# Kernel tuning notes

Measured on AMD Instinct MI355X. Metric: run time of the kernel, lower is better.

The kernel has to match this reference:

```python
import jax, jax.numpy as jnp
import numpy as np

H, D, BS = 32, 128, 64          # num_heads, head_dim, gate block_size
GATE_DIM = 64
GATE_TEMP = 2.0                 # _GATE_TARGET_TEMPERATURE
CLAMP_MIN, CLAMP_MAX = -50.0, 50.0


def _rotate_half(x):
    x1, x2 = jnp.split(x, 2, axis=-1)
    return jnp.concatenate([-x2, x1], axis=-1)


def setup_inputs() -> dict:
    key = jax.random.key(0)
    ks = jax.random.split(key, 8)
    B, S, E = 1, 2048, 4096
    hidden_states = jax.random.normal(ks[0], (B, S, E), jnp.float32) * 0.02
    # standard RoPE tables, [B, S, D]
    inv_freq = 1.0 / (10000.0 ** (jnp.arange(0, D, 2, dtype=jnp.float32) / D))
    freqs = jnp.arange(S, dtype=jnp.float32)[:, None] * inv_freq[None, :]
    emb = jnp.concatenate([freqs, freqs], axis=-1)
    cos = jnp.broadcast_to(jnp.cos(emb)[None], (B, S, D)).astype(jnp.float32)
    sin = jnp.broadcast_to(jnp.sin(emb)[None], (B, S, D)).astype(jnp.float32)
    Wq = jax.random.normal(ks[1], (E, E), jnp.float32) * 0.02
    Wk = jax.random.normal(ks[2], (E, E), jnp.float32) * 0.02
    Wv = jax.random.normal(ks[3], (E, E), jnp.float32) * 0.02
    Wo = jax.random.normal(ks[4], (E, E), jnp.float32) * 0.02
    Wg_q = jax.random.normal(ks[5], (GATE_DIM, D), jnp.float32) * 0.05
    Wg_k = jax.random.normal(ks[6], (GATE_DIM, D), jnp.float32) * 0.05
    return {"hidden_states": hidden_states, "cos": cos, "sin": sin,
            "Wq": Wq, "Wk": Wk, "Wv": Wv, "Wo": Wo,
            "Wg_q": Wg_q, "Wg_k": Wg_k}


def reference(hidden_states, cos, sin, Wq, Wk, Wv, Wo, Wg_q, Wg_k):
    B, S, E = hidden_states.shape
    scale = np.float32(1.0 / np.sqrt(D))

    # ---- base attention (training path: full dense attention w/ scores) ----
    q = (hidden_states @ Wq.T).reshape(B, S, H, D).transpose(0, 2, 1, 3)  # [B,H,S,D]
    k = (hidden_states @ Wk.T).reshape(B, S, H, D).transpose(0, 2, 1, 3)
    v = (hidden_states @ Wv.T).reshape(B, S, H, D).transpose(0, 2, 1, 3)

    # _apply_rotary_pos_emb: cos/sin are 3D [B,S,D] -> unsqueeze head dim
    c, s = cos[:, None], sin[:, None]
    q = q * c + _rotate_half(q) * s
    k = k * c + _rotate_half(k) * s

    scores = jnp.einsum('bhqd,bhkd->bhqk', q, k) * scale  # [B,H,S,S]
    causal = jnp.tril(jnp.ones((S, S), dtype=bool))
    scores = jnp.where(causal, scores, -jnp.inf)
    attn = jax.nn.softmax(scores, axis=-1)
    ctx = jnp.einsum('bhqk,bhkd->bhqd', attn, v)
    attn_output = ctx.transpose(0, 2, 1, 3).reshape(B, S, E) @ Wo.T

    # ---- _compute_gate_target: blockwise maxpool -> clamp -> tempered softmax ----
    NB = S // BS  # S divisible by BS, so the -inf padding branch is a no-op
    block_max = scores.reshape(B, H, NB, BS, NB, BS).max(axis=(3, 5))  # [B,H,NB,NB]
    finite = jnp.isfinite(block_max)
    block_max = jnp.where(finite, jnp.clip(block_max, CLAMP_MIN, CLAMP_MAX), block_max)
    gate_target = jax.nn.softmax(
        block_max.reshape(B, H, NB * NB) / GATE_TEMP, axis=-1
    ).reshape(B, H, NB, NB)

    # ---- AttnGate prediction: mean-pooled block Q/K -> low-rank block logits ----
    qb = q.reshape(B, H, NB, BS, D).mean(axis=3)  # [B,H,NB,D]
    kb = k.reshape(B, H, NB, BS, D).mean(axis=3)
    gq = jnp.einsum('bhnd,gd->bhng', qb, Wg_q)
    gk = jnp.einsum('bhnd,gd->bhng', kb, Wg_k)
    glogits = jnp.einsum('bhqg,bhkg->bhqk', gq, gk) * np.float32(1.0 / np.sqrt(GATE_DIM))
    bmask = jnp.tril(jnp.ones((NB, NB), dtype=bool))  # block-causal
    glogits = jnp.where(bmask, glogits, -jnp.inf)
    gate_pred = jax.nn.softmax(
        glogits.reshape(B, H, NB * NB), axis=-1
    ).reshape(B, H, NB, NB)

    return attn_output, gate_pred, gate_target
```

## Files before the change

### kernel.cpp

```cpp
#include <hip/hip_runtime.h>
#include <stdint.h>

#define S_LEN 2048
#define EMB   4096
#define NHEAD 32
#define DHEAD 128
#define NBLK  32
#define GDIM  64

typedef float  f32x4  __attribute__((ext_vector_type(4)));
typedef __bf16 bf16x8 __attribute__((ext_vector_type(8)));
typedef unsigned short u16;

__device__ __forceinline__ u16 f2bf(float f) {
  uint32_t u = __float_as_uint(f);
  u += 0x7fffu + ((u >> 16) & 1u);
  return (u16)(u >> 16);
}
__device__ __forceinline__ float bf2f(u16 u) {
  return __uint_as_float(((uint32_t)u) << 16);
}

__device__ __forceinline__ void ld_lds16(const u16* g, u16* l) {
  __builtin_amdgcn_global_load_lds((const __attribute__((address_space(1))) void*)g,
                                   (__attribute__((address_space(3))) void*)l, 16, 0, 0);
}

__global__ void conv_f32_bf16(const float* __restrict__ in, u16* __restrict__ out, int n4) {
  int i = blockIdx.x * 256 + threadIdx.x;
  if (i >= n4) return;
  float4 v = ((const float4*)in)[i];
  ushort4 o;
  o.x = f2bf(v.x); o.y = f2bf(v.y); o.z = f2bf(v.z); o.w = f2bf(v.w);
  ((ushort4*)out)[i] = o;
}

template<int MODE>
__global__ void __launch_bounds__(256, 2) gemm_bt(
    const u16* __restrict__ A, const u16* __restrict__ B, void* __restrict__ outp,
    const float* __restrict__ cosp, const float* __restrict__ sinp)
{
  __shared__ u16 lA[128 * 32];
  __shared__ u16 lB[128 * 32];
  __shared__ u16 lT[MODE == 1 ? 128 * 136 : 1];

  const int tid = threadIdx.x;
  const int w = tid >> 6, lane = tid & 63;
  const int r = lane & 15, qd = lane >> 4;
  const int m0 = blockIdx.y * 128, n0 = blockIdx.x * 128;
  const int K = EMB;

  f32x4 acc[2][8];
#pragma unroll
  for (int mi = 0; mi < 2; ++mi)
#pragma unroll
    for (int ni = 0; ni < 8; ++ni) acc[mi][ni] = (f32x4){0.f, 0.f, 0.f, 0.f};

  const u16* Ab = A + (size_t)(m0 + w * 16 + (lane >> 2)) * K + (lane & 3) * 8;
  const u16* Bb = B + (size_t)(n0 + w * 16 + (lane >> 2)) * K + (lane & 3) * 8;
  u16* lAb = &lA[(w * 16) * 32];
  u16* lBb = &lB[(w * 16) * 32];

  for (int k0 = 0; k0 < K; k0 += 32) {
    __syncthreads();
    ld_lds16(Ab + k0, lAb);
    ld_lds16(Ab + (size_t)64 * K + k0, lAb + 64 * 32);
    ld_lds16(Bb + k0, lBb);
    ld_lds16(Bb + (size_t)64 * K + k0, lBb + 64 * 32);
    __syncthreads();
    bf16x8 af0 = *(const bf16x8*)&lA[(w * 32 + r) * 32 + qd * 8];
    bf16x8 af1 = *(const bf16x8*)&lA[(w * 32 + 16 + r) * 32 + qd * 8];
#pragma unroll
    for (int ni = 0; ni < 8; ++ni) {
      bf16x8 bf = *(const bf16x8*)&lB[(ni * 16 + r) * 32 + qd * 8];
      acc[0][ni] = __builtin_amdgcn_mfma_f32_16x16x32_bf16(af0, bf, acc[0][ni], 0, 0, 0);
      acc[1][ni] = __builtin_amdgcn_mfma_f32_16x16x32_bf16(af1, bf, acc[1][ni], 0, 0, 0);
    }
  }

  if (MODE == 2) {
    float* out = (float*)outp;
#pragma unroll
    for (int mi = 0; mi < 2; ++mi)
#pragma unroll
      for (int ni = 0; ni < 8; ++ni)
#pragma unroll
        for (int rg = 0; rg < 4; ++rg) {
          int srow = m0 + w * 32 + mi * 16 + qd * 4 + rg;
          out[(size_t)srow * EMB + n0 + ni * 16 + r] = acc[mi][ni][rg];
        }
  } else if (MODE == 0) {
    u16* out = (u16*)outp;
    const int h = n0 >> 7;
#pragma unroll
    for (int mi = 0; mi < 2; ++mi)
#pragma unroll
      for (int ni = 0; ni < 4; ++ni)
#pragma unroll
        for (int rg = 0; rg < 4; ++rg) {
          int srow = m0 + w * 32 + mi * 16 + qd * 4 + rg;
          int dlo = ni * 16 + r;
          float c = cosp[srow * DHEAD + dlo];
          float s = sinp[srow * DHEAD + dlo];
          float lo = acc[mi][ni][rg], hi = acc[mi][ni + 4][rg];
          size_t base = ((size_t)h * S_LEN + srow) * DHEAD;
          out[base + dlo]      = f2bf(lo * c - hi * s);
          out[base + dlo + 64] = f2bf(hi * c + lo * s);
        }
  } else {
    u16* out = (u16*)outp;
    const int h = n0 >> 7;
#pragma unroll
    for (int mi = 0; mi < 2; ++mi)
#pragma unroll
      for (int ni = 0; ni < 8; ++ni)
#pragma unroll
        for (int rg = 0; rg < 4; ++rg) {
          int sl = w * 32 + mi * 16 + qd * 4 + rg;
          lT[sl * 136 + ni * 16 + r] = f2bf(acc[mi][ni][rg]);
        }
    __syncthreads();
    const int d = tid >> 1, sh = (tid & 1) * 64;
    size_t obase = ((size_t)h * DHEAD + d) * S_LEN + m0 + sh;
#pragma unroll
    for (int i8 = 0; i8 < 8; ++i8) {
      u16 tmp[8];
#pragma unroll
      for (int j = 0; j < 8; ++j) tmp[j] = lT[(sh + i8 * 8 + j) * 136 + d];
      *(uint4*)&out[obase + i8 * 8] = *(uint4*)tmp;
    }
  }
}

__global__ void __launch_bounds__(256, 2) attn_fwd(
    const u16* __restrict__ qg, const u16* __restrict__ kg, const u16* __restrict__ vtg,
    u16* __restrict__ ctx, float* __restrict__ bmax)
{
  __shared__ u16 lK[64 * 136];
  __shared__ u16 lV[128 * 72];
  __shared__ u16 lP[64 * 72];
  __shared__ float lBM[4 * NBLK];

  const int tid = threadIdx.x;
  const int w = tid >> 6, lane = tid & 63;
  const int r = lane & 15, qd = lane >> 4;
  const int qb = blockIdx.x, h = blockIdx.y;

  bf16x8 qf[4];
  {
    const u16* qp = qg + ((size_t)h * S_LEN + qb * 64 + w * 16 + r) * DHEAD + qd * 8;
#pragma unroll
    for (int ki = 0; ki < 4; ++ki) qf[ki] = *(const bf16x8*)(qp + ki * 32);
  }

  f32x4 o[8];
#pragma unroll
  for (int dt = 0; dt < 8; ++dt) o[dt] = (f32x4){0.f, 0.f, 0.f, 0.f};
  float m_run[4], l_run[4];
#pragma unroll
  for (int rg = 0; rg < 4; ++rg) { m_run[rg] = -__builtin_inff(); l_run[rg] = 0.f; }

  const u16* ksrc = kg + (size_t)h * S_LEN * DHEAD;
  const u16* vsrc = vtg + (size_t)h * DHEAD * S_LEN;
  const float scale = 0.08838834764831845f;

  for (int kb = 0; kb <= qb; ++kb) {
    __syncthreads();
#pragma unroll
    for (int i = 0; i < 4; ++i) {
      int c = tid + 256 * i;
      int row = c >> 4, col = (c & 15) * 8;
      *(uint4*)&lK[row * 136 + col] = *(const uint4*)(ksrc + (size_t)(kb * 64 + row) * DHEAD + col);
    }
#pragma unroll
    for (int i = 0; i < 4; ++i) {
      int c = tid + 256 * i;
      int row = c >> 3, col = (c & 7) * 8;
      *(uint4*)&lV[row * 72 + col] = *(const uint4*)(vsrc + (size_t)row * S_LEN + kb * 64 + col);
    }
    __syncthreads();

    f32x4 sf[4];
#pragma unroll
    for (int nt = 0; nt < 4; ++nt) sf[nt] = (f32x4){0.f, 0.f, 0.f, 0.f};
#pragma unroll
    for (int ki = 0; ki < 4; ++ki)
#pragma unroll
      for (int nt = 0; nt < 4; ++nt) {
        bf16x8 bf = *(const bf16x8*)&lK[(nt * 16 + r) * 136 + ki * 32 + qd * 8];
        sf[nt] = __builtin_amdgcn_mfma_f32_16x16x32_bf16(qf[ki], bf, sf[nt], 0, 0, 0);
      }

    float rmax[4];
#pragma unroll
    for (int rg = 0; rg < 4; ++rg) rmax[rg] = -__builtin_inff();
#pragma unroll
    for (int nt = 0; nt < 4; ++nt)
#pragma unroll
      for (int rg = 0; rg < 4; ++rg) {
        float s = sf[nt][rg] * scale;
        if (kb == qb) {
          int col = nt * 16 + r, row = w * 16 + qd * 4 + rg;
          if (col > row) s = -__builtin_inff();
        }
        sf[nt][rg] = s;
        rmax[rg] = fmaxf(rmax[rg], s);
      }
#pragma unroll
    for (int rg = 0; rg < 4; ++rg) {
      float v = rmax[rg];
      v = fmaxf(v, __shfl_xor(v, 1));
      v = fmaxf(v, __shfl_xor(v, 2));
      v = fmaxf(v, __shfl_xor(v, 4));
      v = fmaxf(v, __shfl_xor(v, 8));
      rmax[rg] = v;
    }
    {
      float v = fmaxf(fmaxf(rmax[0], rmax[1]), fmaxf(rmax[2], rmax[3]));
      v = fmaxf(v, __shfl_xor(v, 16));
      v = fmaxf(v, __shfl_xor(v, 32));
      if (lane == 0) lBM[w * NBLK + kb] = v;
    }

    float alpha[4], rsum[4];
#pragma unroll
    for (int rg = 0; rg < 4; ++rg) {
      float mn = fmaxf(m_run[rg], rmax[rg]);
      alpha[rg] = __expf(m_run[rg] - mn);
      m_run[rg] = mn;
      rsum[rg] = 0.f;
    }
#pragma unroll
    for (int nt = 0; nt < 4; ++nt)
#pragma unroll
      for (int rg = 0; rg < 4; ++rg) {
        float p = __expf(sf[nt][rg] - m_run[rg]);
        sf[nt][rg] = p;
        rsum[rg] += p;
      }
#pragma unroll
    for (int rg = 0; rg < 4; ++rg) {
      float v = rsum[rg];
      v += __shfl_xor(v, 1);
      v += __shfl_xor(v, 2);
      v += __shfl_xor(v, 4);
      v += __shfl_xor(v, 8);
      l_run[rg] = l_run[rg] * alpha[rg] + v;
    }
#pragma unroll
    for (int nt = 0; nt < 4; ++nt)
#pragma unroll
      for (int rg = 0; rg < 4; ++rg)
        lP[(w * 16 + qd * 4 + rg) * 72 + nt * 16 + r] = f2bf(sf[nt][rg]);
#pragma unroll
    for (int dt = 0; dt < 8; ++dt)
#pragma unroll
      for (int rg = 0; rg < 4; ++rg) o[dt][rg] *= alpha[rg];
    bf16x8 pa0 = *(const bf16x8*)&lP[(w * 16 + r) * 72 + qd * 8];
    bf16x8 pa1 = *(const bf16x8*)&lP[(w * 16 + r) * 72 + 32 + qd * 8];
#pragma unroll
    for (int dt = 0; dt < 8; ++dt) {
      bf16x8 bv0 = *(const bf16x8*)&lV[(dt * 16 + r) * 72 + qd * 8];
      bf16x8 bv1 = *(const bf16x8*)&lV[(dt * 16 + r) * 72 + 32 + qd * 8];
      o[dt] = __builtin_amdgcn_mfma_f32_16x16x32_bf16(pa0, bv0, o[dt], 0, 0, 0);
      o[dt] = __builtin_amdgcn_mfma_f32_16x16x32_bf16(pa1, bv1, o[dt], 0, 0, 0);
    }
  }

  float inv[4];
#pragma unroll
  for (int rg = 0; rg < 4; ++rg) inv[rg] = 1.f / l_run[rg];
#pragma unroll
  for (int dt = 0; dt < 8; ++dt)
#pragma unroll
    for (int rg = 0; rg < 4; ++rg) {
      int srow = qb * 64 + w * 16 + qd * 4 + rg;
      ctx[(size_t)srow * EMB + h * DHEAD + dt * 16 + r] = f2bf(o[dt][rg] * inv[rg]);
    }
  __syncthreads();
  if (tid <= qb) {
    float v = fmaxf(fmaxf(lBM[0 * NBLK + tid], lBM[1 * NBLK + tid]),
                    fmaxf(lBM[2 * NBLK + tid], lBM[3 * NBLK + tid]));
    bmax[((size_t)h * NBLK + qb) * NBLK + tid] = v;
  }
}

__global__ void bmean(const u16* __restrict__ x, float* __restrict__ out) {
  int nb = blockIdx.x, h = blockIdx.y, d = threadIdx.x;
  const u16* p = x + ((size_t)h * S_LEN + nb * 64) * DHEAD + d;
  float s = 0.f;
#pragma unroll 8
  for (int i = 0; i < 64; ++i) s += bf2f(p[(size_t)i * DHEAD]);
  out[((size_t)h * NBLK + nb) * DHEAD + d] = s * (1.f / 64.f);
}

__global__ void __launch_bounds__(256) gate_kernel(
    const float* __restrict__ qm, const float* __restrict__ km,
    const float* __restrict__ Wgq, const float* __restrict__ Wgk,
    const float* __restrict__ bmx, float* __restrict__ gpred, float* __restrict__ gtgt)
{
  __shared__ float gq[NBLK * GDIM], gk[NBLK * GDIM];
  __shared__ float red[256];
  const int h = blockIdx.x, tid = threadIdx.x;

  for (int i = 0; i < 8; ++i) {
    int e = tid + 256 * i;
    int n = e >> 6, g = e & 63;
    const float* qrow = qm + ((size_t)h * NBLK + n) * DHEAD;
    const float* krow = km + ((size_t)h * NBLK + n) * DHEAD;
    const float* wq = Wgq + g * DHEAD;
    const float* wk = Wgk + g * DHEAD;
    float s1 = 0.f, s2 = 0.f;
    for (int d = 0; d < DHEAD; ++d) { s1 += qrow[d] * wq[d]; s2 += krow[d] * wk[d]; }
    gq[e] = s1; gk[e] = s2;
  }
  __syncthreads();

  float gl[4];
  for (int i = 0; i < 4; ++i) {
    int idx = tid + 256 * i;
    int qn = idx >> 5, kn = idx & 31;
    if (kn <= qn) {
      float s = 0.f;
      for (int g = 0; g < GDIM; ++g) s += gq[qn * GDIM + g] * gk[kn * GDIM + g];
      gl[i] = s * 0.125f;
    } else gl[i] = -__builtin_inff();
  }
  float mx = fmaxf(fmaxf(gl[0], gl[1]), fmaxf(gl[2], gl[3]));
  red[tid] = mx; __syncthreads();
  for (int st = 128; st > 0; st >>= 1) { if (tid < st) red[tid] = fmaxf(red[tid], red[tid + st]); __syncthreads(); }
  float gmax = red[0]; __syncthreads();
  float ex[4], lsum = 0.f;
  for (int i = 0; i < 4; ++i) { ex[i] = __expf(gl[i] - gmax); lsum += ex[i]; }
  red[tid] = lsum; __syncthreads();
  for (int st = 128; st > 0; st >>= 1) { if (tid < st) red[tid] += red[tid + st]; __syncthreads(); }
  float invs = 1.f / red[0]; __syncthreads();
  for (int i = 0; i < 4; ++i) gpred[(size_t)h * 1024 + tid + 256 * i] = ex[i] * invs;

  float tl[4];
  for (int i = 0; i < 4; ++i) {
    int idx = tid + 256 * i;
    int qn = idx >> 5, kn = idx & 31;
    tl[i] = (kn <= qn) ? fminf(fmaxf(bmx[(size_t)h * 1024 + idx], -50.f), 50.f) * 0.5f
                       : -__builtin_inff();
  }
  float mx2 = fmaxf(fmaxf(tl[0], tl[1]), fmaxf(tl[2], tl[3]));
  red[tid] = mx2; __syncthreads();
  for (int st = 128; st > 0; st >>= 1) { if (tid < st) red[tid] = fmaxf(red[tid], red[tid + st]); __syncthreads(); }
  float tmax = red[0]; __syncthreads();
  float ex2[4], ls2 = 0.f;
  for (int i = 0; i < 4; ++i) { ex2[i] = __expf(tl[i] - tmax); ls2 += ex2[i]; }
  red[tid] = ls2; __syncthreads();
  for (int st = 128; st > 0; st >>= 1) { if (tid < st) red[tid] += red[tid + st]; __syncthreads(); }
  float inv2 = 1.f / red[0];
  for (int i = 0; i < 4; ++i) gtgt[(size_t)h * 1024 + tid + 256 * i] = ex2[i] * inv2;
}

extern "C" void kernel_launch(void* const* d_in, const int* in_sizes, int n_in,
                              void* d_out, int out_size, void* d_ws, size_t ws_size,
                              hipStream_t stream) {
  const float* hidden = (const float*)d_in[0];
  const float* cosp   = (const float*)d_in[1];
  const float* sinp   = (const float*)d_in[2];
  const float* Wq     = (const float*)d_in[3];
  const float* Wk     = (const float*)d_in[4];
  const float* Wv     = (const float*)d_in[5];
  const float* Wo     = (const float*)d_in[6];
  const float* Wgq    = (const float*)d_in[7];
  const float* Wgk    = (const float*)d_in[8];

  char* ws = (char*)d_ws;
  u16*   wbuf = (u16*)ws;
  u16*   hid  = (u16*)(ws + 33554432);
  u16*   qbf  = (u16*)(ws + 50331648);
  u16*   kbf  = (u16*)(ws + 67108864);
  u16*   vtb  = (u16*)(ws + 83886080);
  u16*   ctxb = (u16*)(ws + 100663296);
  float* bmx  = (float*)(ws + 117440512);
  float* qmn  = (float*)(ws + 117571584);
  float* kmn  = (float*)(ws + 118095872);

  float* attn_out = (float*)d_out;
  float* gpred = attn_out + (size_t)S_LEN * EMB;
  float* gtgt  = gpred + NHEAD * NBLK * NBLK;

  conv_f32_bf16<<<8192, 256, 0, stream>>>(hidden, hid, 2097152);

  conv_f32_bf16<<<16384, 256, 0, stream>>>(Wq, wbuf, 4194304);
  gemm_bt<0><<<dim3(32, 16), 256, 0, stream>>>(hid, wbuf, qbf, cosp, sinp);
  conv_f32_bf16<<<16384, 256, 0, stream>>>(Wk, wbuf, 4194304);
  gemm_bt<0><<<dim3(32, 16), 256, 0, stream>>>(hid, wbuf, kbf, cosp, sinp);
  conv_f32_bf16<<<16384, 256, 0, stream>>>(Wv, wbuf, 4194304);
  gemm_bt<1><<<dim3(32, 16), 256, 0, stream>>>(hid, wbuf, vtb, nullptr, nullptr);

  attn_fwd<<<dim3(NBLK, NHEAD), 256, 0, stream>>>(qbf, kbf, vtb, ctxb, bmx);

  conv_f32_bf16<<<16384, 256, 0, stream>>>(Wo, wbuf, 4194304);
  gemm_bt<2><<<dim3(32, 16), 256, 0, stream>>>(ctxb, wbuf, attn_out, nullptr, nullptr);

  bmean<<<dim3(NBLK, NHEAD), 128, 0, stream>>>(qbf, qmn);
  bmean<<<dim3(NBLK, NHEAD), 128, 0, stream>>>(kbf, kmn);
  gate_kernel<<<NHEAD, 256, 0, stream>>>(qmn, kmn, Wgq, Wgk, bmx, gpred, gtgt);
}
```

Measured before the change: 901.8 us.

## Fuse QKV GEMMs, batch weight conversion, pair causal attention blocks

Converts Wq/Wk/Wv in one launch and runs a single QKV GEMM grid of 96x16 tiles instead of three separate GEMMs. This removes serialization and tail effects between the smaller launches. Attention now gives each workgroup query blocks qb and 31-qb, which balances causal work across half as many blocks. The change also pads LDS strides differently, merges the two bmean kernels into one vectorized kernel, and reuses d_out and workspace as scratch for weights. That scratch reuse relies on gemm_out overwriting d_out after the Wv buffer is dead.

After: 790.6 us. -12.3%, faster.

```diff
diff --git a/kernel.cpp b/kernel.cpp
--- a/kernel.cpp
+++ b/kernel.cpp
@@ -35,20 +35,37 @@
   ((ushort4*)out)[i] = o;
 }
 
-template<int MODE>
-__global__ void __launch_bounds__(256, 2) gemm_bt(
-    const u16* __restrict__ A, const u16* __restrict__ B, void* __restrict__ outp,
-    const float* __restrict__ cosp, const float* __restrict__ sinp)
+__global__ void conv3_f32_bf16(const float* __restrict__ a, const float* __restrict__ b,
+                               const float* __restrict__ c, u16* __restrict__ oa,
+                               u16* __restrict__ ob, u16* __restrict__ oc, int n4) {
+  int i = blockIdx.x * 256 + threadIdx.x;
+  if (i >= n4) return;
+  const float* in = (blockIdx.y == 0) ? a : (blockIdx.y == 1) ? b : c;
+  u16* out = (blockIdx.y == 0) ? oa : (blockIdx.y == 1) ? ob : oc;
+  float4 v = ((const float4*)in)[i];
+  ushort4 o;
+  o.x = f2bf(v.x); o.y = f2bf(v.y); o.z = f2bf(v.z); o.w = f2bf(v.w);
+  ((ushort4*)out)[i] = o;
+}
+
+__global__ void __launch_bounds__(256, 2) qkv_gemm(
+    const u16* __restrict__ A, const u16* __restrict__ Bq, const u16* __restrict__ Bk,
+    const u16* __restrict__ Bv, u16* __restrict__ outq, u16* __restrict__ outk,
+    u16* __restrict__ outvt, const float* __restrict__ cosp, const float* __restrict__ sinp)
 {
   __shared__ u16 lA[128 * 32];
   __shared__ u16 lB[128 * 32];
-  __shared__ u16 lT[MODE == 1 ? 128 * 136 : 1];
+  __shared__ u16 lT[128 * 132];
 
   const int tid = threadIdx.x;
   const int w = tid >> 6, lane = tid & 63;
   const int r = lane & 15, qd = lane >> 4;
-  const int m0 = blockIdx.y * 128, n0 = blockIdx.x * 128;
+  const int nb = blockIdx.x;
+  const int which = nb >> 5;
+  const int h = nb & 31;
+  const int m0 = blockIdx.y * 128, n0 = h * 128;
   const int K = EMB;
+  const u16* B = (which == 0) ? Bq : (which == 1) ? Bk : Bv;
 
   f32x4 acc[2][8];
 #pragma unroll
@@ -78,20 +95,8 @@
     }
   }
 
-  if (MODE == 2) {
-    float* out = (float*)outp;
-#pragma unroll
-    for (int mi = 0; mi < 2; ++mi)
-#pragma unroll
-      for (int ni = 0; ni < 8; ++ni)
-#pragma unroll
-        for (int rg = 0; rg < 4; ++rg) {
-          int srow = m0 + w * 32 + mi * 16 + qd * 4 + rg;
-          out[(size_t)srow * EMB + n0 + ni * 16 + r] = acc[mi][ni][rg];
-        }
-  } else if (MODE == 0) {
-    u16* out = (u16*)outp;
-    const int h = n0 >> 7;
+  if (which < 2) {
+    u16* out = which ? outk : outq;
 #pragma unroll
     for (int mi = 0; mi < 2; ++mi)
 #pragma unroll
@@ -108,8 +113,6 @@
           out[base + dlo + 64] = f2bf(hi * c + lo * s);
         }
   } else {
-    u16* out = (u16*)outp;
-    const int h = n0 >> 7;
 #pragma unroll
     for (int mi = 0; mi < 2; ++mi)
 #pragma unroll
@@ -117,7 +120,7 @@
 #pragma unroll
         for (int rg = 0; rg < 4; ++rg) {
           int sl = w * 32 + mi * 16 + qd * 4 + rg;
-          lT[sl * 136 + ni * 16 + r] = f2bf(acc[mi][ni][rg]);
+          lT[sl * 132 + ni * 16 + r] = f2bf(acc[mi][ni][rg]);
         }
     __syncthreads();
     const int d = tid >> 1, sh = (tid & 1) * 64;
@@ -126,172 +129,232 @@
     for (int i8 = 0; i8 < 8; ++i8) {
       u16 tmp[8];
 #pragma unroll
-      for (int j = 0; j < 8; ++j) tmp[j] = lT[(sh + i8 * 8 + j) * 136 + d];
-      *(uint4*)&out[obase + i8 * 8] = *(uint4*)tmp;
-    }
-  }
+      for (int j = 0; j < 8; ++j) tmp[j] = lT[(sh + i8 * 8 + j) * 132 + d];
+      *(uint4*)&outvt[obase + i8 * 8] = *(uint4*)tmp;
+    }
+  }
+}
+
+__global__ void __launch_bounds__(256, 2) gemm_out(
+    const u16* __restrict__ A, const u16* __restrict__ B, float* __restrict__ out)
+{
+  __shared__ u16 lA[128 * 32];
+  __shared__ u16 lB[128 * 32];
+  const int tid = threadIdx.x;
+  const int w = tid >> 6, lane = tid & 63;
+  const int r = lane & 15, qd = lane >> 4;
+  const int m0 = blockIdx.y * 128, n0 = blockIdx.x * 128;
+  const int K = EMB;
+
+  f32x4 acc[2][8];
+#pragma unroll
+  for (int mi = 0; mi < 2; ++mi)
+#pragma unroll
+    for (int ni = 0; ni < 8; ++ni) acc[mi][ni] = (f32x4){0.f, 0.f, 0.f, 0.f};
+
+  const u16* Ab = A + (size_t)(m0 + w * 16 + (lane >> 2)) * K + (lane & 3) * 8;
+  const u16* Bb = B + (size_t)(n0 + w * 16 + (lane >> 2)) * K + (lane & 3) * 8;
+  u16* lAb = &lA[(w * 16) * 32];
+  u16* lBb = &lB[(w * 16) * 32];
+
+  for (int k0 = 0; k0 < K; k0 += 32) {
+    __syncthreads();
+    ld_lds16(Ab + k0, lAb);
+    ld_lds16(Ab + (size_t)64 * K + k0, lAb + 64 * 32);
+    ld_lds16(Bb + k0, lBb);
+    ld_lds16(Bb + (size_t)64 * K + k0, lBb + 64 * 32);
+    __syncthreads();
+    bf16x8 af0 = *(const bf16x8*)&lA[(w * 32 + r) * 32 + qd * 8];
+    bf16x8 af1 = *(const bf16x8*)&lA[(w * 32 + 16 + r) * 32 + qd * 8];
+#pragma unroll
+    for (int ni = 0; ni < 8; ++ni) {
+      bf16x8 bf = *(const bf16x8*)&lB[(ni * 16 + r) * 32 + qd * 8];
+      acc[0][ni] = __builtin_amdgcn_mfma_f32_16x16x32_bf16(af0, bf, acc[0][ni], 0, 0, 0);
+      acc[1][ni] = __builtin_amdgcn_mfma_f32_16x16x32_bf16(af1, bf, acc[1][ni], 0, 0, 0);
+    }
+  }
+#pragma unroll
+  for (int mi = 0; mi < 2; ++mi)
+#pragma unroll
+    for (int ni = 0; ni < 8; ++ni)
+#pragma unroll
+      for (int rg = 0; rg < 4; ++rg) {
+        int srow = m0 + w * 32 + mi * 16 + qd * 4 + rg;
+        out[(size_t)srow * EMB + n0 + ni * 16 + r] = acc[mi][ni][rg];
+      }
 }
 
 __global__ void __launch_bounds__(256, 2) attn_fwd(
     const u16* __restrict__ qg, const u16* __restrict__ kg, const u16* __restrict__ vtg,
     u16* __restrict__ ctx, float* __restrict__ bmax)
 {
-  __shared__ u16 lK[64 * 136];
-  __shared__ u16 lV[128 * 72];
-  __shared__ u16 lP[64 * 72];
+  __shared__ u16 lK[64 * 132];
+  __shared__ u16 lV[128 * 76];
+  __shared__ u16 lP[64 * 76];
   __shared__ float lBM[4 * NBLK];
 
   const int tid = threadIdx.x;
   const int w = tid >> 6, lane = tid & 63;
   const int r = lane & 15, qd = lane >> 4;
-  const int qb = blockIdx.x, h = blockIdx.y;
-
-  bf16x8 qf[4];
-  {
-    const u16* qp = qg + ((size_t)h * S_LEN + qb * 64 + w * 16 + r) * DHEAD + qd * 8;
-#pragma unroll
-    for (int ki = 0; ki < 4; ++ki) qf[ki] = *(const bf16x8*)(qp + ki * 32);
-  }
-
-  f32x4 o[8];
-#pragma unroll
-  for (int dt = 0; dt < 8; ++dt) o[dt] = (f32x4){0.f, 0.f, 0.f, 0.f};
-  float m_run[4], l_run[4];
-#pragma unroll
-  for (int rg = 0; rg < 4; ++rg) { m_run[rg] = -__builtin_inff(); l_run[rg] = 0.f; }
-
+  const int h = blockIdx.y;
   const u16* ksrc = kg + (size_t)h * S_LEN * DHEAD;
   const u16* vsrc = vtg + (size_t)h * DHEAD * S_LEN;
   const float scale = 0.08838834764831845f;
 
-  for (int kb = 0; kb <= qb; ++kb) {
-    __syncthreads();
-#pragma unroll
-    for (int i = 0; i < 4; ++i) {
-      int c = tid + 256 * i;
-      int row = c >> 4, col = (c & 15) * 8;
-      *(uint4*)&lK[row * 136 + col] = *(const uint4*)(ksrc + (size_t)(kb * 64 + row) * DHEAD + col);
-    }
-#pragma unroll
-    for (int i = 0; i < 4; ++i) {
-      int c = tid + 256 * i;
-      int row = c >> 3, col = (c & 7) * 8;
-      *(uint4*)&lV[row * 72 + col] = *(const uint4*)(vsrc + (size_t)row * S_LEN + kb * 64 + col);
-    }
-    __syncthreads();
-
-    f32x4 sf[4];
-#pragma unroll
-    for (int nt = 0; nt < 4; ++nt) sf[nt] = (f32x4){0.f, 0.f, 0.f, 0.f};
-#pragma unroll
-    for (int ki = 0; ki < 4; ++ki)
-#pragma unroll
-      for (int nt = 0; nt < 4; ++nt) {
-        bf16x8 bf = *(const bf16x8*)&lK[(nt * 16 + r) * 136 + ki * 32 + qd * 8];
-        sf[nt] = __builtin_amdgcn_mfma_f32_16x16x32_bf16(qf[ki], bf, sf[nt], 0, 0, 0);
-      }
-
-    float rmax[4];
-#pragma unroll
-    for (int rg = 0; rg < 4; ++rg) rmax[rg] = -__builtin_inff();
-#pragma unroll
-    for (int nt = 0; nt < 4; ++nt)
+  for (int qsel = 0; qsel < 2; ++qsel) {
+    const int qb = qsel ? (31 - (int)blockIdx.x) : (int)blockIdx.x;
+
+    bf16x8 qf[4];
+    {
+      const u16* qp = qg + ((size_t)h * S_LEN + qb * 64 + w * 16 + r) * DHEAD + qd * 8;
+#pragma unroll
+      for (int ki = 0; ki < 4; ++ki) qf[ki] = *(const bf16x8*)(qp + ki * 32);
+    }
+
+    f32x4 o[8];
+#pragma unroll
+    for (int dt = 0; dt < 8; ++dt) o[dt] = (f32x4){0.f, 0.f, 0.f, 0.f};
+    float m_run[4], l_run[4];
+#pragma unroll
+    for (int rg = 0; rg < 4; ++rg) { m_run[rg] = -__builtin_inff(); l_run[rg] = 0.f; }
+
+    for (int kb = 0; kb <= qb; ++kb) {
+      __syncthreads();
+#pragma unroll
+      for (int i = 0; i < 4; ++i) {
+        int c = tid + 256 * i;
+        int row = c >> 4, col = (c & 15) * 8;
+        *(uint4*)&lK[row * 132 + col] = *(const uint4*)(ksrc + (size_t)(kb * 64 + row) * DHEAD + col);
+      }
+#pragma unroll
+      for (int i = 0; i < 4; ++i) {
+        int c = tid + 256 * i;
+        int row = c >> 3, col = (c & 7) * 8;
+        *(uint4*)&lV[row * 76 + col] = *(const uint4*)(vsrc + (size_t)row * S_LEN + kb * 64 + col);
+      }
+      __syncthreads();
+
+      f32x4 sf[4];
+#pragma unroll
+      for (int nt = 0; nt < 4; ++nt) sf[nt] = (f32x4){0.f, 0.f, 0.f, 0.f};
+#pragma unroll
+      for (int ki = 0; ki < 4; ++ki)
+#pragma unroll
+        for (int nt = 0; nt < 4; ++nt) {
+          bf16x8 bf = *(const bf16x8*)&lK[(nt * 16 + r) * 132 + ki * 32 + qd * 8];
+          sf[nt] = __builtin_amdgcn_mfma_f32_16x16x32_bf16(qf[ki], bf, sf[nt], 0, 0, 0);
+        }
+
+      float rmax[4];
+#pragma unroll
+      for (int rg = 0; rg < 4; ++rg) rmax[rg] = -__builtin_inff();
+#pragma unroll
+      for (int nt = 0; nt < 4; ++nt)
+#pragma unroll
+        for (int rg = 0; rg < 4; ++rg) {
+          float s = sf[nt][rg] * scale;
+          if (kb == qb) {
+            int col = nt * 16 + r, row = w * 16 + qd * 4 + rg;
+            if (col > row) s = -__builtin_inff();
+          }
+          sf[nt][rg] = s;
+          rmax[rg] = fmaxf(rmax[rg], s);
+        }
 #pragma unroll
       for (int rg = 0; rg < 4; ++rg) {
-        float s = sf[nt][rg] * scale;
-        if (kb == qb) {
-          int col = nt * 16 + r, row = w * 16 + qd * 4 + rg;
-          if (col > row) s = -__builtin_inff();
+        float v = rmax[rg];
+        v = fmaxf(v, __shfl_xor(v, 1));
+        v = fmaxf(v, __shfl_xor(v, 2));
+        v = fmaxf(v, __shfl_xor(v, 4));
+        v = fmaxf(v, __shfl_xor(v, 8));
+        rmax[rg] = v;
+      }
+      {
+        float v = fmaxf(fmaxf(rmax[0], rmax[1]), fmaxf(rmax[2], rmax[3]));
+        v = fmaxf(v, __shfl_xor(v, 16));
+        v = fmaxf(v, __shfl_xor(v, 32));
+        if (lane == 0) lBM[w * NBLK + kb] = v;
+      }
+
+      float alpha[4], rsum[4];
+#pragma unroll
+      for (int rg = 0; rg < 4; ++rg) {
+        float mn = fmaxf(m_run[rg], rmax[rg]);
+        alpha[rg] = __expf(m_run[rg] - mn);
+        m_run[rg] = mn;
+        rsum[rg] = 0.f;
+      }
+#pragma unroll
+      for (int nt = 0; nt < 4; ++nt)
+#pragma unroll
+        for (int rg = 0; rg < 4; ++rg) {
+          float p = __expf(sf[nt][rg] - m_run[rg]);
+          sf[nt][rg] = p;
+          rsum[rg] += p;
         }
-        sf[nt][rg] = s;
-        rmax[rg] = fmaxf(rmax[rg], s);
-      }
-#pragma unroll
-    for (int rg = 0; rg < 4; ++rg) {
-      float v = rmax[rg];
-      v = fmaxf(v, __shfl_xor(v, 1));
-      v = fmaxf(v, __shfl_xor(v, 2));
-      v = fmaxf(v, __shfl_xor(v, 4));
-      v = fmaxf(v, __shfl_xor(v, 8));
-      rmax[rg] = v;
-    }
-    {
-      float v = fmaxf(fmaxf(rmax[0], rmax[1]), fmaxf(rmax[2], rmax[3]));
-      v = fmaxf(v, __shfl_xor(v, 16));
-      v = fmaxf(v, __shfl_xor(v, 32));
-      if (lane == 0) lBM[w * NBLK + kb] = v;
-    }
-
-    float alpha[4], rsum[4];
-#pragma unroll
-    for (int rg = 0; rg < 4; ++rg) {
-      float mn = fmaxf(m_run[rg], rmax[rg]);
-      alpha[rg] = __expf(m_run[rg] - mn);
-      m_run[rg] = mn;
-      rsum[rg] = 0.f;
-    }
-#pragma unroll
-    for (int nt = 0; nt < 4; ++nt)
 #pragma unroll
       for (int rg = 0; rg < 4; ++rg) {
-        float p = __expf(sf[nt][rg] - m_run[rg]);
-        sf[nt][rg] = p;
-        rsum[rg] += p;
-      }
-#pragma unroll
-    for (int rg = 0; rg < 4; ++rg) {
-      float v = rsum[rg];
-      v += __shfl_xor(v, 1);
-      v += __shfl_xor(v, 2);
-      v += __shfl_xor(v, 4);
-      v += __shfl_xor(v, 8);
-      l_run[rg] = l_run[rg] * alpha[rg] + v;
-    }
-#pragma unroll
-    for (int nt = 0; nt < 4; ++nt)
-#pragma unroll
-      for (int rg = 0; rg < 4; ++rg)
-        lP[(w * 16 + qd * 4 + rg) * 72 + nt * 16 + r] = f2bf(sf[nt][rg]);
+        float v = rsum[rg];
+        v += __shfl_xor(v, 1);
+        v += __shfl_xor(v, 2);
+        v += __shfl_xor(v, 4);
+        v += __shfl_xor(v, 8);
+        l_run[rg] = l_run[rg] * alpha[rg] + v;
+      }
+#pragma unroll
+      for (int nt = 0; nt < 4; ++nt)
+#pragma unroll
+        for (int rg = 0; rg < 4; ++rg)
+          lP[(w * 16 + qd * 4 + rg) * 76 + nt * 16 + r] = f2bf(sf[nt][rg]);
+#pragma unroll
+      for (int dt = 0; dt < 8; ++dt)
+#pragma unroll
+        for (int rg = 0; rg < 4; ++rg) o[dt][rg] *= alpha[rg];
+      bf16x8 pa0 = *(const bf16x8*)&lP[(w * 16 + r) * 76 + qd * 8];
+      bf16x8 pa1 = *(const bf16x8*)&lP[(w * 16 + r) * 76 + 32 + qd * 8];
+#pragma unroll
+      for (int dt = 0; dt < 8; ++dt) {
+        bf16x8 bv0 = *(const bf16x8*)&lV[(dt * 16 + r) * 76 + qd * 8];
+        bf16x8 bv1 = *(const bf16x8*)&lV[(dt * 16 + r) * 76 + 32 + qd * 8];
+        o[dt] = __builtin_amdgcn_mfma_f32_16x16x32_bf16(pa0, bv0, o[dt], 0, 0, 0);
+        o[dt] = __builtin_amdgcn_mfma_f32_16x16x32_bf16(pa1, bv1, o[dt], 0, 0, 0);
+      }
+    }
+
+    float inv[4];
+#pragma unroll
+    for (int rg = 0; rg < 4; ++rg) inv[rg] = 1.f / l_run[rg];
 #pragma unroll
     for (int dt = 0; dt < 8; ++dt)
 #pragma unroll
-      for (int rg = 0; rg < 4; ++rg) o[dt][rg] *= alpha[rg];
-    bf16x8 pa0 = *(const bf16x8*)&lP[(w * 16 + r) * 72 + qd * 8];
-    bf16x8 pa1 = *(const bf16x8*)&lP[(w * 16 + r) * 72 + 32 + qd * 8];
-#pragma unroll
-    for (int dt = 0; dt < 8; ++dt) {
-      bf16x8 bv0 = *(const bf16x8*)&lV[(dt * 16 + r) * 72 + qd * 8];
-      bf16x8 bv1 = *(const bf16x8*)&lV[(dt * 16 + r) * 72 + 32 + qd * 8];
-      o[dt] = __builtin_amdgcn_mfma_f32_16x16x32_bf16(pa0, bv0, o[dt], 0, 0, 0);
-      o[dt] = __builtin_amdgcn_mfma_f32_16x16x32_bf16(pa1, bv1, o[dt], 0, 0, 0);
-    }
-  }
-
-  float inv[4];
-#pragma unroll
-  for (int rg = 0; rg < 4; ++rg) inv[rg] = 1.f / l_run[rg];
-#pragma unroll
-  for (int dt = 0; dt < 8; ++dt)
-#pragma unroll
-    for (int rg = 0; rg < 4; ++rg) {
-      int srow = qb * 64 + w * 16 + qd * 4 + rg;
-      ctx[(size_t)srow * EMB + h * DHEAD + dt * 16 + r] = f2bf(o[dt][rg] * inv[rg]);
-    }
-  __syncthreads();
-  if (tid <= qb) {
-    float v = fmaxf(fmaxf(lBM[0 * NBLK + tid], lBM[1 * NBLK + tid]),
-                    fmaxf(lBM[2 * NBLK + tid], lBM[3 * NBLK + tid]));
-    bmax[((size_t)h * NBLK + qb) * NBLK + tid] = v;
-  }
-}
-
-__global__ void bmean(const u16* __restrict__ x, float* __restrict__ out) {
-  int nb = blockIdx.x, h = blockIdx.y, d = threadIdx.x;
-  const u16* p = x + ((size_t)h * S_LEN + nb * 64) * DHEAD + d;
-  float s = 0.f;
+      for (int rg = 0; rg < 4; ++rg) {
+        int srow = qb * 64 + w * 16 + qd * 4 + rg;
+        ctx[(size_t)srow * EMB + h * DHEAD + dt * 16 + r] = f2bf(o[dt][rg] * inv[rg]);
+      }
+    __syncthreads();
+    if (tid <= qb) {
+      float v = fmaxf(fmaxf(lBM[0 * NBLK + tid], lBM[1 * NBLK + tid]),
+                      fmaxf(lBM[2 * NBLK + tid], lBM[3 * NBLK + tid]));
+      bmax[((size_t)h * NBLK + qb) * NBLK + tid] = v;
+    }
+  }
+}
+
+__global__ void bmean2(const u16* __restrict__ q, const u16* __restrict__ k,
+                       float* __restrict__ qo, float* __restrict__ ko) {
+  int nb = blockIdx.x, h = blockIdx.y, t = threadIdx.x;
+  const u16* x = blockIdx.z ? k : q;
+  float* out = blockIdx.z ? ko : qo;
+  const u16* p = x + ((size_t)h * S_LEN + nb * 64) * DHEAD + t * 2;
+  float s0 = 0.f, s1 = 0.f;
 #pragma unroll 8
-  for (int i = 0; i < 64; ++i) s += bf2f(p[(size_t)i * DHEAD]);
-  out[((size_t)h * NBLK + nb) * DHEAD + d] = s * (1.f / 64.f);
+  for (int i = 0; i < 64; ++i) {
+    uint32_t v = *(const uint32_t*)(p + (size_t)i * DHEAD);
+    s0 += bf2f((u16)v);
+    s1 += bf2f((u16)(v >> 16));
+  }
+  float2 rr = {s0 * (1.f / 64.f), s1 * (1.f / 64.f)};
+  *(float2*)&out[((size_t)h * NBLK + nb) * DHEAD + t * 2] = rr;
 }
 
 __global__ void __launch_bounds__(256) gate_kernel(
@@ -370,35 +433,33 @@
   const float* Wgk    = (const float*)d_in[8];
 
   char* ws = (char*)d_ws;
-  u16*   wbuf = (u16*)ws;
-  u16*   hid  = (u16*)(ws + 33554432);
-  u16*   qbf  = (u16*)(ws + 50331648);
-  u16*   kbf  = (u16*)(ws + 67108864);
-  u16*   vtb  = (u16*)(ws + 83886080);
-  u16*   ctxb = (u16*)(ws + 100663296);
-  float* bmx  = (float*)(ws + 117440512);
-  float* qmn  = (float*)(ws + 117571584);
-  float* kmn  = (float*)(ws + 118095872);
+  u16* wqb = (u16*)ws;
+  u16* wkb = (u16*)(ws + 33554432);
+  u16* hid = (u16*)(ws + 67108864);
+  u16* qbf = (u16*)(ws + 83886080);
+  u16* kbf = (u16*)(ws + 100663296);
+  u16* vtb = (u16*)(ws + 117440512);
+  float* bmx = (float*)(ws + 33554432);
+  float* qmn = (float*)(ws + 33554432 + 131072);
+  float* kmn = (float*)(ws + 33554432 + 655360);
+  u16* ctx = hid;
+  u16* wvb = (u16*)d_out;
 
   float* attn_out = (float*)d_out;
   float* gpred = attn_out + (size_t)S_LEN * EMB;
   float* gtgt  = gpred + NHEAD * NBLK * NBLK;
 
+  conv3_f32_bf16<<<dim3(16384, 3), 256, 0, stream>>>(Wq, Wk, Wv, wqb, wkb, wvb, 4194304);
   conv_f32_bf16<<<8192, 256, 0, stream>>>(hidden, hid, 2097152);
 
-  conv_f32_bf16<<<16384, 256, 0, stream>>>(Wq, wbuf, 4194304);
-  gemm_bt<0><<<dim3(32, 16), 256, 0, stream>>>(hid, wbuf, qbf, cosp, sinp);
-  conv_f32_bf16<<<16384, 256, 0, stream>>>(Wk, wbuf, 4194304);
-  gemm_bt<0><<<dim3(32, 16), 256, 0, stream>>>(hid, wbuf, kbf, cosp, sinp);
-  conv_f32_bf16<<<16384, 256, 0, stream>>>(Wv, wbuf, 4194304);
-  gemm_bt<1><<<dim3(32, 16), 256, 0, stream>>>(hid, wbuf, vtb, nullptr, nullptr);
-
-  attn_fwd<<<dim3(NBLK, NHEAD), 256, 0, stream>>>(qbf, kbf, vtb, ctxb, bmx);
-
-  conv_f32_bf16<<<16384, 256, 0, stream>>>(Wo, wbuf, 4194304);
-  gemm_bt<2><<<dim3(32, 16), 256, 0, stream>>>(ctxb, wbuf, attn_out, nullptr, nullptr);
-
-  bmean<<<dim3(NBLK, NHEAD), 128, 0, stream>>>(qbf, qmn);
-  bmean<<<dim3(NBLK, NHEAD), 128, 0, stream>>>(kbf, kmn);
+  qkv_gemm<<<dim3(96, 16), 256, 0, stream>>>(hid, wqb, wkb, wvb, qbf, kbf, vtb, cosp, sinp);
+
+  conv_f32_bf16<<<16384, 256, 0, stream>>>(Wo, wqb, 4194304);
+
+  attn_fwd<<<dim3(16, NHEAD), 256, 0, stream>>>(qbf, kbf, vtb, ctx, bmx);
+
+  bmean2<<<dim3(NBLK, NHEAD, 2), 128, 0, stream>>>(qbf, kbf, qmn, kmn);
   gate_kernel<<<NHEAD, 256, 0, stream>>>(qmn, kmn, Wgq, Wgk, bmx, gpred, gtgt);
-}
+
+  gemm_out<<<dim3(32, 16), 256, 0, stream>>>(ctx, wqb, attn_out);
+}
```
